# Performance work log

Measured on AMD Instinct MI355X. Metric: run time of the kernel, lower is better.

The kernel has to match this reference:

```python
import jax, jax.numpy as jnp
import numpy as np
from jax import lax

K = 32          # num_units (ring size / channels)
T = 100         # num_iters
FAR, NEAR = 29, 9
RING_MIN, RING_MAX, RING_BW = -0.5, 0.1, 0.5
NEAR_SUM = FAR_SUM = 0.4
H_STEP, TAU, DECAY_K = 1.0, 5.0, 1.0   # step_size, time_constant, decay_constant


def _ring_weight():
    # FeatureConnections._kernel: min-max-scaled gaussian bump, rolled per out-channel.
    X = np.linspace(0.0, 1.0, K)
    base = np.exp(-0.5 * ((X - X[K // 2]) / RING_BW) ** 2)  # pdf normalization cancels in min-max
    base = (base - base.min()) / (base.max() - base.min())
    base = base * (RING_MAX - RING_MIN) + RING_MIN
    W = np.stack([np.roll(base, K // 2 + i) for i in range(K)])  # (K_out, K_in)
    return W.astype(np.float32)


def _surround_kernel():
    # SpatialConnections._kernel: near excitation, far inhibition (opponent surround).
    inh = -FAR_SUM / (FAR ** 2 - NEAR ** 2)
    exc = NEAR_SUM / NEAR ** 2
    k = np.full((FAR, FAR), inh, dtype=np.float32)
    u = FAR // 2 - NEAR // 2
    v = FAR // 2 + NEAR // 2 + 1
    k[u:v, u:v] = exc
    return k


def setup_inputs() -> dict:
    key = jax.random.key(0)
    k1, k2, k3 = jax.random.split(key, 3)
    inbound = jax.random.normal(k1, (2, K, 64, 64), dtype=jnp.float32)
    Wf = jnp.asarray(_ring_weight())                                   # (K, K) 1x1 channel mixing
    bf = jax.random.normal(k2, (K,), dtype=jnp.float32) * 0.01        # Conv2d bias (random init in source)
    Ws = jnp.asarray(np.broadcast_to(_surround_kernel(), (K, FAR, FAR)).copy())  # diagonal (depthwise) taps
    bs = jax.random.normal(k3, (K,), dtype=jnp.float32) * 0.01
    return {"inbound": inbound, "Wf": Wf, "bf": bf, "Ws": Ws, "bs": bs}


def reference(inbound, Wf, bf, Ws, bs):
    decay = 1.0 - H_STEP * DECAY_K ** 2 / TAU   # 0.8
    gain = H_STEP / TAU                          # 0.2
    dw = Ws[:, None]                             # (K, 1, FAR, FAR) depthwise kernel (diag of full KxK conv)

    def feat(X):  # 1x1 ring-attractor channel mix
        return jnp.einsum('oi,nihw->nohw', Wf, X) + bf[None, :, None, None]

    def spat(X):  # depthwise opponent-surround conv, 'SAME' == padding (FAR-1)//2
        y = lax.conv_general_dilated(X, dw, (1, 1), 'SAME',
                                     dimension_numbers=('NCHW', 'OIHW', 'NCHW'),
                                     feature_group_count=K)
        return y + bs[None, :, None, None]

    drive = 0.5 * inbound

    def step(X, _):
        S = drive + feat(X) + spat(X)
        Xn = decay * X + gain * jax.nn.relu(S)
        return Xn, Xn

    X0 = jnp.zeros_like(inbound)
    _, Xt = lax.scan(step, X0, None, length=T)   # (T, N, K, H, W)
    return jnp.transpose(Xt, (1, 0, 2, 3, 4))    # (N, T, K, H, W)
```

## Files before the change

### kernel.cpp

```cpp
#include <hip/hip_runtime.h>

#define NN 2
#define KC 32
#define G  4
#define CG (KC/G)
#define TT 100
#define HH 64
#define WW 64
#define HWSZ (HH*WW)
#define RB 4
#define RROWS 16
#define HALO 14
#define BROWS (RROWS + 2*HALO)
#define SW 65
#define TSZ (BROWS*SW)
#define NWG (NN*CG*RB)
#define FLAG_STRIDE 16

typedef float fx4 __attribute__((ext_vector_type(4)));

#define GLD1(x, p) \
  asm volatile("global_load_dwordx4 %0, %1, off sc0 sc1" : "=&v"(x) : "v"(p) : "memory")
#define GLD8(x0,x1,x2,x3,x4,x5,x6,x7,p0,p1,p2,p3,p4,p5,p6,p7) \
  asm volatile( \
    "global_load_dwordx4 %0, %8, off sc0 sc1\n\t" \
    "global_load_dwordx4 %1, %9, off sc0 sc1\n\t" \
    "global_load_dwordx4 %2, %10, off sc0 sc1\n\t" \
    "global_load_dwordx4 %3, %11, off sc0 sc1\n\t" \
    "global_load_dwordx4 %4, %12, off sc0 sc1\n\t" \
    "global_load_dwordx4 %5, %13, off sc0 sc1\n\t" \
    "global_load_dwordx4 %6, %14, off sc0 sc1\n\t" \
    "global_load_dwordx4 %7, %15, off sc0 sc1" \
    : "=&v"(x0),"=&v"(x1),"=&v"(x2),"=&v"(x3), \
      "=&v"(x4),"=&v"(x5),"=&v"(x6),"=&v"(x7) \
    : "v"(p0),"v"(p1),"v"(p2),"v"(p3),"v"(p4),"v"(p5),"v"(p6),"v"(p7) \
    : "memory")
#define VWAIT8(x0,x1,x2,x3,x4,x5,x6,x7) \
  asm volatile("s_waitcnt vmcnt(0)" \
    : "+v"(x0),"+v"(x1),"+v"(x2),"+v"(x3),"+v"(x4),"+v"(x5),"+v"(x6),"+v"(x7) :: "memory")
#define VWAIT11(x0,x1,x2,x3,x4,x5,x6,x7,x8,x9,x10) \
  asm volatile("s_waitcnt vmcnt(0)" \
    : "+v"(x0),"+v"(x1),"+v"(x2),"+v"(x3),"+v"(x4),"+v"(x5), \
      "+v"(x6),"+v"(x7),"+v"(x8),"+v"(x9),"+v"(x10) :: "memory")
#define GST4(p, v) \
  asm volatile("global_store_dwordx4 %0, %1, off sc0 sc1" :: "v"(p), "v"(v) : "memory")

#define BAR_LDS()  asm volatile("s_waitcnt lgkmcnt(0)\n\ts_barrier" ::: "memory")
#define BAR_ONLY() asm volatile("s_barrier" ::: "memory")
#define BAR_FULL() asm volatile("s_waitcnt vmcnt(0) lgkmcnt(0)\n\ts_barrier" ::: "memory")
#define LGKM0()    asm volatile("s_waitcnt lgkmcnt(0)" ::: "memory")

__global__ void __launch_bounds__(256, 1) ring_kernel(
    const float* __restrict__ inbound, const float* __restrict__ Wf,
    const float* __restrict__ bf, const float* __restrict__ Ws,
    const float* __restrict__ bs, float* __restrict__ out,
    unsigned* __restrict__ flags)
{
  __shared__ float T[G*TSZ];
  __shared__ fx4   WFS[KC];

  const int b    = blockIdx.x;
  const int n    = b >> 5;
  const int cg   = (b >> 2) & (CG-1);
  const int rb   = b & (RB-1);
  const int tid  = threadIdx.x;
  const int lane = tid & 63;
  const int wave = tid >> 6;
  const int r0   = rb * RROWS;
  const int ch0  = cg * G;

  const float inh = Ws[0];
  const float exc = Ws[14*29 + 14];
  const float w9  = exc - inh;

  if (tid < KC) {
    fx4 wv;
    wv[0] = Wf[(ch0+0)*KC + tid]; wv[1] = Wf[(ch0+1)*KC + tid];
    wv[2] = Wf[(ch0+2)*KC + tid]; wv[3] = Wf[(ch0+3)*KC + tid];
    WFS[tid] = wv;
  }
  BAR_LDS();

  const int off = r0*WW + tid*4;
  const int rl  = tid >> 4;
  const int w0  = (tid & 15) * 4;
  const int br  = rl + HALO;

  fx4 base[G];
  #pragma unroll
  for (int j = 0; j < G; ++j) {
    const float* dp = inbound + (size_t)(n*KC + ch0 + j)*HWSZ + off;
    float bsum = bf[ch0+j] + bs[ch0+j];
    base[j][0] = 0.5f*dp[0] + bsum; base[j][1] = 0.5f*dp[1] + bsum;
    base[j][2] = 0.5f*dp[2] + bsum; base[j][3] = 0.5f*dp[3] + bsum;
  }

  int  sgofs[11], slofs[11]; bool sval[11];
  #pragma unroll
  for (int q = 0; q < 11; ++q) {
    int id  = lane + 64*q;
    int row = id >> 4;
    int c4  = (id & 15) * 4;
    int g   = r0 - HALO + row;
    sval[q]  = (g >= 0 && g < HH);
    int gc   = g < 0 ? 0 : (g > HH-1 ? HH-1 : g);
    sgofs[q] = gc*WW + c4;
    slofs[q] = row*SW + c4;
  }
  float* Tw = T + wave*TSZ;

  const int ownf = ((n<<5) | (cg<<2) | rb) * FLAG_STRIDE;
  int pollf = ownf;
  if (tid < CG)                  pollf = ((n<<5) | (tid<<2) | rb)    * FLAG_STRIDE;
  else if (tid == 8 && rb>0)     pollf = ((n<<5) | (cg<<2) | (rb-1)) * FLAG_STRIDE;
  else if (tid == 9 && rb<RB-1)  pollf = ((n<<5) | (cg<<2) | (rb+1)) * FLAG_STRIDE;
  unsigned* pollp = flags + pollf;
  unsigned* ownp  = flags + ownf;

  fx4 xn[G];
  #pragma unroll
  for (int j = 0; j < G; ++j) xn[j] = fx4{0.f,0.f,0.f,0.f};

  for (int t = 0; t < TT; ++t) {
    fx4 sf[G], acc[G];
    #pragma unroll
    for (int j = 0; j < G; ++j) { sf[j] = fx4{0,0,0,0}; acc[j] = fx4{0,0,0,0}; }

    if (t > 0) {
      const float* Xprev = out + (size_t)((n*TT + (t-1))*KC)*HWSZ;

      if (tid < 10) {
        const unsigned tgt = (unsigned)t;
        while (__hip_atomic_load(pollp, __ATOMIC_RELAXED, __HIP_MEMORY_SCOPE_AGENT) < tgt) {
          __builtin_amdgcn_s_sleep(1);
        }
      }
      BAR_ONLY();

      fx4 A0,A1,A2,A3,A4,A5,A6,A7, B0,B1,B2,B3,B4,B5,B6,B7;
      const float* Xp = Xprev + off;

      {
        const float* Xc = Xprev + (size_t)(ch0 + wave)*HWSZ;
        fx4 h0,h1,h2,h3,h4,h5,h6,h7,h8,h9,h10;
        GLD1(h0,(const fx4*)(Xc+sgofs[0]));  GLD1(h1,(const fx4*)(Xc+sgofs[1]));
        GLD1(h2,(const fx4*)(Xc+sgofs[2]));  GLD1(h3,(const fx4*)(Xc+sgofs[3]));
        GLD1(h4,(const fx4*)(Xc+sgofs[4]));  GLD1(h5,(const fx4*)(Xc+sgofs[5]));
        GLD1(h6,(const fx4*)(Xc+sgofs[6]));  GLD1(h7,(const fx4*)(Xc+sgofs[7]));
        GLD1(h8,(const fx4*)(Xc+sgofs[8]));  GLD1(h9,(const fx4*)(Xc+sgofs[9]));
        GLD1(h10,(const fx4*)(Xc+sgofs[10]));
        GLD8(A0,A1,A2,A3,A4,A5,A6,A7,
          (const fx4*)(Xp+(size_t)0*HWSZ),(const fx4*)(Xp+(size_t)1*HWSZ),
          (const fx4*)(Xp+(size_t)2*HWSZ),(const fx4*)(Xp+(size_t)3*HWSZ),
          (const fx4*)(Xp+(size_t)4*HWSZ),(const fx4*)(Xp+(size_t)5*HWSZ),
          (const fx4*)(Xp+(size_t)6*HWSZ),(const fx4*)(Xp+(size_t)7*HWSZ));
        GLD8(B0,B1,B2,B3,B4,B5,B6,B7,
          (const fx4*)(Xp+(size_t)8*HWSZ),(const fx4*)(Xp+(size_t)9*HWSZ),
          (const fx4*)(Xp+(size_t)10*HWSZ),(const fx4*)(Xp+(size_t)11*HWSZ),
          (const fx4*)(Xp+(size_t)12*HWSZ),(const fx4*)(Xp+(size_t)13*HWSZ),
          (const fx4*)(Xp+(size_t)14*HWSZ),(const fx4*)(Xp+(size_t)15*HWSZ));
        VWAIT11(h0,h1,h2,h3,h4,h5,h6,h7,h8,h9,h10);
        fx4 hh[11] = {h0,h1,h2,h3,h4,h5,h6,h7,h8,h9,h10};
        #pragma unroll
        for (int q = 0; q < 11; ++q) {
          fx4 v = sval[q] ? hh[q] : fx4{0.f,0.f,0.f,0.f};
          Tw[slofs[q]+0]=v[0]; Tw[slofs[q]+1]=v[1];
          Tw[slofs[q]+2]=v[2]; Tw[slofs[q]+3]=v[3];
        }
      }

      if (lane < BROWS) {
        float* Tr = Tw + lane*SW;
        float a = 0.f;
        #pragma unroll 8
        for (int cc = 0; cc < WW; ++cc) { a += Tr[cc]; Tr[cc] = a; }
      }
      LGKM0();
      {
        float* Tc = Tw + lane;
        float a = 0.f;
        #pragma unroll 4
        for (int r = 0; r < BROWS; ++r) { a += Tc[r*SW]; Tc[r*SW] = a; }
      }
      BAR_LDS();

      #pragma unroll
      for (int j = 0; j < G; ++j) {
        const float* Tj = T + j*TSZ;
        #pragma unroll
        for (int jj = 0; jj < 4; ++jj) {
          int w = w0 + jj;
          int hi  = br + 14, lo  = br - 15;
          int whi = (w + 14 > 63) ? 63 : (w + 14);
          int wlo = w - 15;
          float b29 = Tj[hi*SW + whi];
          if (wlo >= 0) b29 -= Tj[hi*SW + wlo];
          if (lo  >= 0) { b29 -= Tj[lo*SW + whi]; if (wlo >= 0) b29 += Tj[lo*SW + wlo]; }
          int hi2  = br + 4, lo2 = br - 5;
          int whi2 = (w + 4 > 63) ? 63 : (w + 4);
          int wlo2 = w - 5;
          float b9 = Tj[hi2*SW + whi2];
          if (wlo2 >= 0) b9 -= Tj[hi2*SW + wlo2];
          b9 -= Tj[lo2*SW + whi2];
          if (wlo2 >= 0) b9 += Tj[lo2*SW + wlo2];
          sf[j][jj] = inh*b29 + w9*b9;
        }
      }

      #define ACC4(V, i) do { fx4 wv = WFS[i]; \
        acc[0] += wv[0]*(V); acc[1] += wv[1]*(V); \
        acc[2] += wv[2]*(V); acc[3] += wv[3]*(V); } while (0)
      VWAIT8(A0,A1,A2,A3,A4,A5,A6,A7);
      VWAIT8(B0,B1,B2,B3,B4,B5,B6,B7);
      ACC4(A0,0);  ACC4(A1,1);  ACC4(A2,2);  ACC4(A3,3);
      ACC4(A4,4);  ACC4(A5,5);  ACC4(A6,6);  ACC4(A7,7);
      GLD8(A0,A1,A2,A3,A4,A5,A6,A7,
        (const fx4*)(Xp+(size_t)16*HWSZ),(const fx4*)(Xp+(size_t)17*HWSZ),
        (const fx4*)(Xp+(size_t)18*HWSZ),(const fx4*)(Xp+(size_t)19*HWSZ),
        (const fx4*)(Xp+(size_t)20*HWSZ),(const fx4*)(Xp+(size_t)21*HWSZ),
        (const fx4*)(Xp+(size_t)22*HWSZ),(const fx4*)(Xp+(size_t)23*HWSZ));
      ACC4(B0,8);  ACC4(B1,9);  ACC4(B2,10); ACC4(B3,11);
      ACC4(B4,12); ACC4(B5,13); ACC4(B6,14); ACC4(B7,15);
      GLD8(B0,B1,B2,B3,B4,B5,B6,B7,
        (const fx4*)(Xp+(size_t)24*HWSZ),(const fx4*)(Xp+(size_t)25*HWSZ),
        (const fx4*)(Xp+(size_t)26*HWSZ),(const fx4*)(Xp+(size_t)27*HWSZ),
        (const fx4*)(Xp+(size_t)28*HWSZ),(const fx4*)(Xp+(size_t)29*HWSZ),
        (const fx4*)(Xp+(size_t)30*HWSZ),(const fx4*)(Xp+(size_t)31*HWSZ));
      VWAIT8(A0,A1,A2,A3,A4,A5,A6,A7);
      VWAIT8(B0,B1,B2,B3,B4,B5,B6,B7);
      ACC4(A0,16); ACC4(A1,17); ACC4(A2,18); ACC4(A3,19);
      ACC4(A4,20); ACC4(A5,21); ACC4(A6,22); ACC4(A7,23);
      ACC4(B0,24); ACC4(B1,25); ACC4(B2,26); ACC4(B3,27);
      ACC4(B4,28); ACC4(B5,29); ACC4(B6,30); ACC4(B7,31);
      #undef ACC4
    }

    float* ob = out + (size_t)((n*TT + t)*KC)*HWSZ + off;
    #pragma unroll
    for (int j = 0; j < G; ++j) {
      fx4 S = base[j] + sf[j] + acc[j];
      fx4 v;
      v[0] = 0.8f*xn[j][0] + 0.2f*fmaxf(S[0], 0.f);
      v[1] = 0.8f*xn[j][1] + 0.2f*fmaxf(S[1], 0.f);
      v[2] = 0.8f*xn[j][2] + 0.2f*fmaxf(S[2], 0.f);
      v[3] = 0.8f*xn[j][3] + 0.2f*fmaxf(S[3], 0.f);
      xn[j] = v;
      GST4((fx4*)(ob + (size_t)(ch0+j)*HWSZ), v);
    }

    if (t < TT-1) {
      BAR_FULL();
      if (tid == 0) {
        __hip_atomic_store(ownp, (unsigned)(t+1), __ATOMIC_RELAXED,
                           __HIP_MEMORY_SCOPE_AGENT);
      }
    }
  }
}

extern "C" void kernel_launch(void* const* d_in, const int* in_sizes, int n_in,
                              void* d_out, int out_size, void* d_ws, size_t ws_size,
                              hipStream_t stream) {
  const float* inbound = (const float*)d_in[0];
  const float* Wf      = (const float*)d_in[1];
  const float* bf      = (const float*)d_in[2];
  const float* Ws      = (const float*)d_in[3];
  const float* bs      = (const float*)d_in[4];
  float* out = (float*)d_out;
  unsigned* flags = (unsigned*)d_ws;

  hipMemsetAsync(d_ws, 0, NWG*FLAG_STRIDE*sizeof(unsigned), stream);

  void* args[] = {(void*)&inbound, (void*)&Wf, (void*)&bf, (void*)&Ws,
                  (void*)&bs, (void*)&out, (void*)&flags};
  hipLaunchCooperativeKernel((void*)ring_kernel, dim3(NWG), dim3(256),
                             args, 0, stream);
}
```

Measured before the change: 997.9 us.

## Reuse own tile from registers and replace serial row scan with DPP scan

Each workgroup's own 16 interior rows are now written into the LDS tile from the register-resident previous state, with row prefix sums computed before the flag wait. Only the 28 halo rows are loaded from global memory. The serial per-lane 64-column row scan is replaced by a 16-lane DPP inclusive scan across float4 chunks. This cuts global halo traffic, shortens the serial LDS scan, and moves part of the work ahead of the inter-workgroup sync. In exchange it adds an LDS barrier wait where there was a plain barrier, and relies on DPP row_shr with bound_ctrl giving zeros at the row edges.

New measurement: 920.9 us. 1.08x faster.

```diff
diff --git a/kernel.cpp b/kernel.cpp
--- a/kernel.cpp
+++ b/kernel.cpp
@@ -12,6 +12,7 @@
 #define RROWS 16
 #define HALO 14
 #define BROWS (RROWS + 2*HALO)
+#define HROWS (2*HALO)
 #define SW 65
 #define TSZ (BROWS*SW)
 #define NWG (NN*CG*RB)
@@ -35,20 +36,31 @@
       "=&v"(x4),"=&v"(x5),"=&v"(x6),"=&v"(x7) \
     : "v"(p0),"v"(p1),"v"(p2),"v"(p3),"v"(p4),"v"(p5),"v"(p6),"v"(p7) \
     : "memory")
+#define VWAIT7(x0,x1,x2,x3,x4,x5,x6) \
+  asm volatile("s_waitcnt vmcnt(0)" \
+    : "+v"(x0),"+v"(x1),"+v"(x2),"+v"(x3),"+v"(x4),"+v"(x5),"+v"(x6) :: "memory")
 #define VWAIT8(x0,x1,x2,x3,x4,x5,x6,x7) \
   asm volatile("s_waitcnt vmcnt(0)" \
     : "+v"(x0),"+v"(x1),"+v"(x2),"+v"(x3),"+v"(x4),"+v"(x5),"+v"(x6),"+v"(x7) :: "memory")
-#define VWAIT11(x0,x1,x2,x3,x4,x5,x6,x7,x8,x9,x10) \
-  asm volatile("s_waitcnt vmcnt(0)" \
-    : "+v"(x0),"+v"(x1),"+v"(x2),"+v"(x3),"+v"(x4),"+v"(x5), \
-      "+v"(x6),"+v"(x7),"+v"(x8),"+v"(x9),"+v"(x10) :: "memory")
 #define GST4(p, v) \
   asm volatile("global_store_dwordx4 %0, %1, off sc0 sc1" :: "v"(p), "v"(v) : "memory")
 
 #define BAR_LDS()  asm volatile("s_waitcnt lgkmcnt(0)\n\ts_barrier" ::: "memory")
-#define BAR_ONLY() asm volatile("s_barrier" ::: "memory")
 #define BAR_FULL() asm volatile("s_waitcnt vmcnt(0) lgkmcnt(0)\n\ts_barrier" ::: "memory")
 #define LGKM0()    asm volatile("s_waitcnt lgkmcnt(0)" ::: "memory")
+
+template<int CTRL>
+__device__ __forceinline__ float dpp_shr(float x) {
+  return __int_as_float(__builtin_amdgcn_update_dpp(
+      0, __float_as_int(x), CTRL, 0xF, 0xF, true));
+}
+__device__ __forceinline__ float scan16(float s) {
+  s += dpp_shr<0x111>(s);
+  s += dpp_shr<0x112>(s);
+  s += dpp_shr<0x114>(s);
+  s += dpp_shr<0x118>(s);
+  return s;
+}
 
 __global__ void __launch_bounds__(256, 1) ring_kernel(
     const float* __restrict__ inbound, const float* __restrict__ Wf,
@@ -95,17 +107,18 @@
     base[j][2] = 0.5f*dp[2] + bsum; base[j][3] = 0.5f*dp[3] + bsum;
   }
 
-  int  sgofs[11], slofs[11]; bool sval[11];
+  int  sgofs[7], slofs[7]; bool sval[7];
   #pragma unroll
-  for (int q = 0; q < 11; ++q) {
-    int id  = lane + 64*q;
-    int row = id >> 4;
-    int c4  = (id & 15) * 4;
-    int g   = r0 - HALO + row;
+  for (int q = 0; q < 7; ++q) {
+    int id   = lane + 64*q;
+    int hrow = id >> 4;
+    int trow = hrow < HALO ? hrow : hrow + RROWS;
+    int c4   = (id & 15) * 4;
+    int g    = r0 - HALO + trow;
     sval[q]  = (g >= 0 && g < HH);
     int gc   = g < 0 ? 0 : (g > HH-1 ? HH-1 : g);
     sgofs[q] = gc*WW + c4;
-    slofs[q] = row*SW + c4;
+    slofs[q] = trow*SW + c4;
   }
   float* Tw = T + wave*TSZ;
 
@@ -129,26 +142,36 @@
     if (t > 0) {
       const float* Xprev = out + (size_t)((n*TT + (t-1))*KC)*HWSZ;
 
+      {
+        const int mo = br*SW + w0;
+        #pragma unroll
+        for (int j = 0; j < G; ++j) {
+          fx4 v = xn[j];
+          float l0 = v[0], l1 = l0+v[1], l2 = l1+v[2], l3 = l2+v[3];
+          float ex = scan16(l3) - l3;
+          float* Tr = T + j*TSZ + mo;
+          Tr[0]=ex+l0; Tr[1]=ex+l1; Tr[2]=ex+l2; Tr[3]=ex+l3;
+        }
+      }
+
       if (tid < 10) {
         const unsigned tgt = (unsigned)t;
         while (__hip_atomic_load(pollp, __ATOMIC_RELAXED, __HIP_MEMORY_SCOPE_AGENT) < tgt) {
           __builtin_amdgcn_s_sleep(1);
         }
       }
-      BAR_ONLY();
+      BAR_LDS();
 
       fx4 A0,A1,A2,A3,A4,A5,A6,A7, B0,B1,B2,B3,B4,B5,B6,B7;
       const float* Xp = Xprev + off;
 
       {
         const float* Xc = Xprev + (size_t)(ch0 + wave)*HWSZ;
-        fx4 h0,h1,h2,h3,h4,h5,h6,h7,h8,h9,h10;
+        fx4 h0,h1,h2,h3,h4,h5,h6;
         GLD1(h0,(const fx4*)(Xc+sgofs[0]));  GLD1(h1,(const fx4*)(Xc+sgofs[1]));
         GLD1(h2,(const fx4*)(Xc+sgofs[2]));  GLD1(h3,(const fx4*)(Xc+sgofs[3]));
         GLD1(h4,(const fx4*)(Xc+sgofs[4]));  GLD1(h5,(const fx4*)(Xc+sgofs[5]));
-        GLD1(h6,(const fx4*)(Xc+sgofs[6]));  GLD1(h7,(const fx4*)(Xc+sgofs[7]));
-        GLD1(h8,(const fx4*)(Xc+sgofs[8]));  GLD1(h9,(const fx4*)(Xc+sgofs[9]));
-        GLD1(h10,(const fx4*)(Xc+sgofs[10]));
+        GLD1(h6,(const fx4*)(Xc+sgofs[6]));
         GLD8(A0,A1,A2,A3,A4,A5,A6,A7,
           (const fx4*)(Xp+(size_t)0*HWSZ),(const fx4*)(Xp+(size_t)1*HWSZ),
           (const fx4*)(Xp+(size_t)2*HWSZ),(const fx4*)(Xp+(size_t)3*HWSZ),
@@ -159,22 +182,18 @@
           (const fx4*)(Xp+(size_t)10*HWSZ),(const fx4*)(Xp+(size_t)11*HWSZ),
           (const fx4*)(Xp+(size_t)12*HWSZ),(const fx4*)(Xp+(size_t)13*HWSZ),
           (const fx4*)(Xp+(size_t)14*HWSZ),(const fx4*)(Xp+(size_t)15*HWSZ));
-        VWAIT11(h0,h1,h2,h3,h4,h5,h6,h7,h8,h9,h10);
-        fx4 hh[11] = {h0,h1,h2,h3,h4,h5,h6,h7,h8,h9,h10};
+        VWAIT7(h0,h1,h2,h3,h4,h5,h6);
+        fx4 hh[7] = {h0,h1,h2,h3,h4,h5,h6};
         #pragma unroll
-        for (int q = 0; q < 11; ++q) {
+        for (int q = 0; q < 7; ++q) {
           fx4 v = sval[q] ? hh[q] : fx4{0.f,0.f,0.f,0.f};
-          Tw[slofs[q]+0]=v[0]; Tw[slofs[q]+1]=v[1];
-          Tw[slofs[q]+2]=v[2]; Tw[slofs[q]+3]=v[3];
-        }
-      }
-
-      if (lane < BROWS) {
-        float* Tr = Tw + lane*SW;
-        float a = 0.f;
-        #pragma unroll 8
-        for (int cc = 0; cc < WW; ++cc) { a += Tr[cc]; Tr[cc] = a; }
-      }
+          float l0 = v[0], l1 = l0+v[1], l2 = l1+v[2], l3 = l2+v[3];
+          float ex = scan16(l3) - l3;
+          float* Tr = Tw + slofs[q];
+          Tr[0]=ex+l0; Tr[1]=ex+l1; Tr[2]=ex+l2; Tr[3]=ex+l3;
+        }
+      }
+
       LGKM0();
       {
         float* Tc = Tw + lane;
```
